# Kernel optimization log

Hardware: AMD Instinct MI355X
Metric: run time of the kernel (lower is better)

Reference implementation:

```python
import jax, jax.numpy as jnp
import numpy as np

B, T, N, D = 2, 16, 512, 256
HID, HEADS = 256, 8
HD = HID // HEADS // 2  # 16
SCALE = HD ** -0.5
LAMBDA_INIT = 0.8 - 0.6 * float(np.exp(-0.3 * (2 - 1)))  # layer_idx = 2
LN_EPS = 1e-5


def setup_inputs() -> dict:
    key = jax.random.key(0)
    ks = jax.random.split(key, 8)
    return {
        "x": jax.random.normal(ks[0], (B, T, N, D), dtype=jnp.float32),
        "Wq": jax.random.normal(ks[1], (D, HID), dtype=jnp.float32) * (D ** -0.5),
        "Wk": jax.random.normal(ks[2], (D, HID), dtype=jnp.float32) * (D ** -0.5),
        "Wv": jax.random.normal(ks[3], (D, HID), dtype=jnp.float32) * (D ** -0.5),
        "lq1": jax.random.normal(ks[4], (HD,), dtype=jnp.float32) * 0.1,
        "lk1": jax.random.normal(ks[5], (HD,), dtype=jnp.float32) * 0.1,
        "lq2": jax.random.normal(ks[6], (HD,), dtype=jnp.float32) * 0.1,
        "lk2": jax.random.normal(ks[7], (HD,), dtype=jnp.float32) * 0.1,
        "ln_gamma": jnp.ones((2 * HD,), dtype=jnp.float32),
        "ln_beta": jnp.zeros((2 * HD,), dtype=jnp.float32),
    }


def _attn_pair(q, k, v1, v2):
    # q,k,v*: [BT, N, H, HD]; shared softmax applied to both value halves
    p = jax.nn.softmax(jnp.einsum('bnhd,bmhd->bhnm', q, k) * SCALE, axis=-1)
    o1 = jnp.einsum('bhnm,bmhd->bnhd', p, v1)
    o2 = jnp.einsum('bhnm,bmhd->bnhd', p, v2)
    return jnp.concatenate([o1, o2], axis=-1)  # [BT, N, H, 2*HD]


def reference(x, Wq, Wk, Wv, lq1, lk1, lq2, lk2, ln_gamma, ln_beta):
    b, t, n, d = x.shape
    # 1x1 Conv2d over channel dim == per-token linear projection
    q = jnp.einsum('btnd,dh->btnh', x, Wq).reshape(b * t, n, HEADS, 2 * HD)
    k = jnp.einsum('btnd,dh->btnh', x, Wk).reshape(b * t, n, HEADS, 2 * HD)
    v = jnp.einsum('btnd,dh->btnh', x, Wv).reshape(b * t, n, HEADS, 2 * HD)
    q1, q2 = jnp.split(q, 2, axis=-1)
    k1, k2 = jnp.split(k, 2, axis=-1)
    v1, v2 = jnp.split(v, 2, axis=-1)
    attn1 = _attn_pair(q1, k1, v1, v2)
    attn2 = _attn_pair(q2, k2, v1, v2)
    lam = jnp.exp(jnp.sum(lq1 * lk1)) - jnp.exp(jnp.sum(lq2 * lk2)) + LAMBDA_INIT
    y = attn1 - lam * attn2  # [BT, N, H, 2*HD]
    mu = jnp.mean(y, axis=-1, keepdims=True)
    var = jnp.mean(jnp.square(y - mu), axis=-1, keepdims=True)
    y = (y - mu) * jax.lax.rsqrt(var + LN_EPS) * ln_gamma + ln_beta
    y = y * (1.0 - LAMBDA_INIT)
    return y.reshape(b, t, n, HEADS * 2 * HD)
```

## Files before the change

kernel.cpp:

```cpp
#include <hip/hip_runtime.h>
#include <cmath>

typedef unsigned short u16;
typedef unsigned int   u32;
typedef __attribute__((ext_vector_type(8))) short short8;
typedef __attribute__((ext_vector_type(4))) float f32x4;

constexpr int BT    = 32;
constexpr int NTOK  = 512;
constexpr int DIM   = 256;
constexpr int HID   = 256;
constexpr int M_ROWS = BT * NTOK;
constexpr int HM     = M_ROWS * 32;
constexpr size_t TENS = (size_t)M_ROWS * HID;
constexpr float LAMBDA_INIT  = 0.35550906759096927f;
constexpr float ONE_MINUS_LI = 0.6444909324090307f;
constexpr float LN_EPS = 1e-5f;
constexpr float QSCALE = 0.36067376022224085f;

constexpr int KCHUNK = 128;

#define MFMA16(a, b, c) __builtin_amdgcn_mfma_f32_16x16x32_bf16((a), (b), (c), 0, 0, 0)
#define LDS_FENCE() asm volatile("" ::: "memory")

__device__ __forceinline__ u16 f2bf(float f) {
    u32 u = __float_as_uint(f);
    return (u16)((u + 0x7FFFu + ((u >> 16) & 1u)) >> 16);
}

__device__ __forceinline__ float fexp2(float x) {
#if defined(__has_builtin) && __has_builtin(__builtin_amdgcn_exp2f)
    return __builtin_amdgcn_exp2f(x);
#else
    return exp2f(x);
#endif
}

__device__ __forceinline__ u32 pack_bf16(float a, float b) {
    u32 ua = __float_as_uint(a) + 0x8000u;
    u32 ub = __float_as_uint(b) + 0x8000u;
    return __builtin_amdgcn_perm(ub, ua, 0x07060302u);
}

__global__ __launch_bounds__(256) void prep_w(const float* __restrict__ Wq,
                                              const float* __restrict__ Wk,
                                              const float* __restrict__ Wv,
                                              u16* __restrict__ Wt) {
    const float* W = (blockIdx.z == 0) ? Wq : (blockIdx.z == 1) ? Wk : Wv;
    u16* dst = Wt + (size_t)blockIdx.z * 65536;
    __shared__ float T[64][65];
    const int k0 = blockIdx.x * 64, n0 = blockIdx.y * 64;
    const int tr = threadIdx.x >> 4;
    const int tc = threadIdx.x & 15;
    #pragma unroll
    for (int i = 0; i < 4; ++i) {
        int row = tr + i * 16;
        float4 v = *(const float4*)&W[(size_t)(k0 + row) * HID + n0 + tc * 4];
        T[row][tc * 4 + 0] = v.x; T[row][tc * 4 + 1] = v.y;
        T[row][tc * 4 + 2] = v.z; T[row][tc * 4 + 3] = v.w;
    }
    __syncthreads();
    #pragma unroll
    for (int i = 0; i < 4; ++i) {
        int n = tr + i * 16;
        int k4 = tc * 4;
        uint2 pk;
        pk.x = (u32)f2bf(T[k4 + 0][n]) | ((u32)f2bf(T[k4 + 1][n]) << 16);
        pk.y = (u32)f2bf(T[k4 + 2][n]) | ((u32)f2bf(T[k4 + 3][n]) << 16);
        *(uint2*)&dst[(size_t)(n0 + n) * DIM + k0 + k4] = pk;
    }
}

__global__ __launch_bounds__(256, 3) void proj_kernel(
    const float* __restrict__ x, const u16* __restrict__ Wt,
    u16* __restrict__ Qh, u16* __restrict__ Kh, u16* __restrict__ Vh)
{
    __shared__ u16 As[64 * 72];
    __shared__ u16 Bs[3][64 * 72];

    const int tid  = threadIdx.x;
    const int m0   = blockIdx.x * 64;
    const int n0   = blockIdx.y * 64;
    const int lane = tid & 63;
    const int wv   = tid >> 6;
    const int q16  = lane & 15;
    const int quad = lane >> 4;
    const int mw   = (wv >> 1) * 32;
    const int nw   = (wv & 1) * 32;

    const int sr = tid >> 2;
    const int sc = (tid & 3) * 16;

    f32x4 acc[3][4];
    #pragma unroll
    for (int z = 0; z < 3; ++z)
        #pragma unroll
        for (int t = 0; t < 4; ++t)
            acc[z][t] = (f32x4){0.f, 0.f, 0.f, 0.f};

    for (int kk = 0; kk < DIM; kk += 64) {
        {
            const float4* xs = (const float4*)&x[(size_t)(m0 + sr) * DIM + kk + sc];
            float4 g0 = xs[0], g1 = xs[1], g2 = xs[2], g3 = xs[3];
            uint4 o0, o1;
            o0.x = (u32)f2bf(g0.x) | ((u32)f2bf(g0.y) << 16);
            o0.y = (u32)f2bf(g0.z) | ((u32)f2bf(g0.w) << 16);
            o0.z = (u32)f2bf(g1.x) | ((u32)f2bf(g1.y) << 16);
            o0.w = (u32)f2bf(g1.z) | ((u32)f2bf(g1.w) << 16);
            o1.x = (u32)f2bf(g2.x) | ((u32)f2bf(g2.y) << 16);
            o1.y = (u32)f2bf(g2.z) | ((u32)f2bf(g2.w) << 16);
            o1.z = (u32)f2bf(g3.x) | ((u32)f2bf(g3.y) << 16);
            o1.w = (u32)f2bf(g3.z) | ((u32)f2bf(g3.w) << 16);
            *(uint4*)&As[sr * 72 + sc]     = o0;
            *(uint4*)&As[sr * 72 + sc + 8] = o1;
        }
        #pragma unroll
        for (int z = 0; z < 3; ++z) {
            const uint4* ws4 = (const uint4*)&Wt[(size_t)z * 65536 + (size_t)(n0 + sr) * DIM + kk + sc];
            *(uint4*)&Bs[z][sr * 72 + sc]     = ws4[0];
            *(uint4*)&Bs[z][sr * 72 + sc + 8] = ws4[1];
        }
        __syncthreads();
        #pragma unroll
        for (int kc = 0; kc < 2; ++kc) {
            short8 a0 = *(const short8*)&As[(mw +      q16) * 72 + kc * 32 + quad * 8];
            short8 a1 = *(const short8*)&As[(mw + 16 + q16) * 72 + kc * 32 + quad * 8];
            #pragma unroll
            for (int z = 0; z < 3; ++z) {
                short8 b0 = *(const short8*)&Bs[z][(nw +      q16) * 72 + kc * 32 + quad * 8];
                short8 b1 = *(const short8*)&Bs[z][(nw + 16 + q16) * 72 + kc * 32 + quad * 8];
                acc[z][0] = MFMA16(a0, b0, acc[z][0]);
                acc[z][1] = MFMA16(a0, b1, acc[z][1]);
                acc[z][2] = MFMA16(a1, b0, acc[z][2]);
                acc[z][3] = MFMA16(a1, b1, acc[z][3]);
            }
        }
        __syncthreads();
    }

    const int hcol = (n0 + nw) >> 5;
    #pragma unroll
    for (int z = 0; z < 3; ++z) {
        u16* C = (z == 0) ? Qh : (z == 1) ? Kh : Vh;
        u16* base = C + (size_t)hcol * HM;
        const float s = (z == 0) ? QSCALE : 1.0f;
        #pragma unroll
        for (int r = 0; r < 4; ++r) {
            const int row = m0 + mw + quad * 4 + r;
            base[(size_t)row * 32 + q16]             = f2bf(acc[z][0][r] * s);
            base[(size_t)row * 32 + q16 + 16]        = f2bf(acc[z][1][r] * s);
            base[(size_t)(row + 16) * 32 + q16]      = f2bf(acc[z][2][r] * s);
            base[(size_t)(row + 16) * 32 + q16 + 16] = f2bf(acc[z][3][r] * s);
        }
    }
}

__global__ __launch_bounds__(256, 3) void attn_kernel(
    const u16* __restrict__ Qh, const u16* __restrict__ Kh, const u16* __restrict__ Vh,
    const float* __restrict__ lq1, const float* __restrict__ lk1,
    const float* __restrict__ lq2, const float* __restrict__ lk2,
    const float* __restrict__ gamma, const float* __restrict__ beta,
    float* __restrict__ out)
{
    constexpr int VSTR = KCHUNK + 8;
    constexpr int NKC  = KCHUNK / 32;

    __shared__ u16 Ks[KCHUNK * 40];
    __shared__ u16 Vts[32 * VSTR];
    __shared__ u16 Pbuf[4][2][2][16 * 40];

    const int qh  = blockIdx.x;
    const int h   = blockIdx.y;
    const int bt  = blockIdx.z;
    const int tid = threadIdx.x;
    const int lane = tid & 63;
    const int wv   = tid >> 6;
    const int q16  = lane & 15;
    const int quad = lane >> 4;

    float sa = 0.f, sb = 0.f;
    #pragma unroll
    for (int d = 0; d < 16; ++d) { sa += lq1[d] * lk1[d]; sb += lq2[d] * lk2[d]; }
    const float lam = __expf(sa) - __expf(sb) + LAMBDA_INIT;

    short8 qv[2];
    #pragma unroll
    for (int qbi = 0; qbi < 2; ++qbi) {
        const int qrow = bt * NTOK + qh * 128 + (qbi * 4 + wv) * 16 + q16;
        qv[qbi] = *(const short8*)(Qh + (size_t)h * HM + (size_t)qrow * 32 + quad * 8);
    }

    const short8 z8 = {0, 0, 0, 0, 0, 0, 0, 0};
    const f32x4  z4 = {0.f, 0.f, 0.f, 0.f};
    const short8 ones8 = {(short)0x3F80, (short)0x3F80, (short)0x3F80, (short)0x3F80,
                          (short)0x3F80, (short)0x3F80, (short)0x3F80, (short)0x3F80};

    f32x4 o1lo[2], o1hi[2], o2lo[2], o2hi[2];
    f32x4 accl1[2], accl2[2];
    #pragma unroll
    for (int qbi = 0; qbi < 2; ++qbi) {
        o1lo[qbi] = z4; o1hi[qbi] = z4; o2lo[qbi] = z4; o2hi[qbi] = z4;
        accl1[qbi] = z4; accl2[qbi] = z4;
    }

    for (int chunk = 0; chunk < NTOK / KCHUNK; ++chunk) {
        if (chunk) __syncthreads();
        {
            const int key  = tid >> 1;
            const int half = (tid & 1) * 16;
            const uint4* src = (const uint4*)(Kh + (size_t)h * HM +
                                (size_t)(bt * NTOK + chunk * KCHUNK + key) * 32 + half);
            uint4* dst = (uint4*)&Ks[key * 40 + half];
            dst[0] = src[0]; dst[1] = src[1];
        }
        {
            const int pr = tid >> 2;
            const int qd = tid & 3;
            const int j0 = pr * 2;
            const u16* v0 = Vh + (size_t)h * HM + (size_t)(bt * NTOK + chunk * KCHUNK + j0) * 32;
            union U { uint4 q4; u32 w[4]; } ra, rb;
            ra.q4 = ((const uint4*)v0)[qd];
            rb.q4 = ((const uint4*)(v0 + 32))[qd];
            #pragma unroll
            for (int k = 0; k < 4; ++k) {
                const int w = qd * 4 + k;
                u32 lo = __builtin_amdgcn_perm(rb.w[k], ra.w[k], 0x05040100u);
                u32 hi = __builtin_amdgcn_perm(rb.w[k], ra.w[k], 0x07060302u);
                *(u32*)&Vts[(2 * w)     * VSTR + j0] = lo;
                *(u32*)&Vts[(2 * w + 1) * VSTR + j0] = hi;
            }
        }
        __syncthreads();

        #pragma unroll
        for (int qbi = 0; qbi < 2; ++qbi) {
            const short8 A1 = (lane < 32) ? qv[qbi] : z8;
            const short8 A2 = (lane < 32) ? z8 : qv[qbi];

            #pragma unroll
            for (int kc = 0; kc < NKC; ++kc) {
                #pragma unroll
                for (int sub = 0; sub < 2; ++sub) {
                    const int key0 = kc * 32 + sub * 16;
                    short8 kf = *(const short8*)&Ks[(key0 + q16) * 40 + quad * 8];
                    __builtin_amdgcn_s_setprio(1);
                    f32x4 s1 = MFMA16(kf, A1, z4);
                    f32x4 s2 = MFMA16(kf, A2, z4);
                    __builtin_amdgcn_s_setprio(0);
                    float p0 = fexp2(s1[0]), p1 = fexp2(s1[1]);
                    float p2 = fexp2(s1[2]), p3 = fexp2(s1[3]);
                    uint2 w1; w1.x = pack_bf16(p0, p1); w1.y = pack_bf16(p2, p3);
                    *(uint2*)&Pbuf[wv][kc & 1][0][q16 * 40 + sub * 16 + quad * 4] = w1;
                    float r0 = fexp2(s2[0]), r1 = fexp2(s2[1]);
                    float r2 = fexp2(s2[2]), r3 = fexp2(s2[3]);
                    uint2 w2; w2.x = pack_bf16(r0, r1); w2.y = pack_bf16(r2, r3);
                    *(uint2*)&Pbuf[wv][kc & 1][1][q16 * 40 + sub * 16 + quad * 4] = w2;
                }
                LDS_FENCE();
                if (kc > 0) {
                    const int pk = kc - 1;
                    const int pb = (kc - 1) & 1;
                    short8 pf1 = *(const short8*)&Pbuf[wv][pb][0][q16 * 40 + quad * 8];
                    short8 pf2 = *(const short8*)&Pbuf[wv][pb][1][q16 * 40 + quad * 8];
                    short8 vlo = *(const short8*)&Vts[q16        * VSTR + pk * 32 + quad * 8];
                    short8 vhi = *(const short8*)&Vts[(16 + q16) * VSTR + pk * 32 + quad * 8];
                    __builtin_amdgcn_s_setprio(1);
                    o1lo[qbi] = MFMA16(pf1, vlo, o1lo[qbi]);
                    o1hi[qbi] = MFMA16(pf1, vhi, o1hi[qbi]);
                    o2lo[qbi] = MFMA16(pf2, vlo, o2lo[qbi]);
                    o2hi[qbi] = MFMA16(pf2, vhi, o2hi[qbi]);
                    accl1[qbi] = MFMA16(pf1, ones8, accl1[qbi]);
                    accl2[qbi] = MFMA16(pf2, ones8, accl2[qbi]);
                    __builtin_amdgcn_s_setprio(0);
                }
                LDS_FENCE();
            }
            {
                const int pk = NKC - 1;
                const int pb = (NKC - 1) & 1;
                short8 pf1 = *(const short8*)&Pbuf[wv][pb][0][q16 * 40 + quad * 8];
                short8 pf2 = *(const short8*)&Pbuf[wv][pb][1][q16 * 40 + quad * 8];
                short8 vlo = *(const short8*)&Vts[q16        * VSTR + pk * 32 + quad * 8];
                short8 vhi = *(const short8*)&Vts[(16 + q16) * VSTR + pk * 32 + quad * 8];
                __builtin_amdgcn_s_setprio(1);
                o1lo[qbi] = MFMA16(pf1, vlo, o1lo[qbi]);
                o1hi[qbi] = MFMA16(pf1, vhi, o1hi[qbi]);
                o2lo[qbi] = MFMA16(pf2, vlo, o2lo[qbi]);
                o2hi[qbi] = MFMA16(pf2, vhi, o2hi[qbi]);
                accl1[qbi] = MFMA16(pf1, ones8, accl1[qbi]);
                accl2[qbi] = MFMA16(pf2, ones8, accl2[qbi]);
                __builtin_amdgcn_s_setprio(0);
            }
            LDS_FENCE();
        }
    }

    const float g_lo = gamma[q16],      g_hi = gamma[16 + q16];
    const float b_lo = beta[q16],       b_hi = beta[16 + q16];

    #pragma unroll
    for (int qbi = 0; qbi < 2; ++qbi) {
        #pragma unroll
        for (int r = 0; r < 4; ++r) {
            const float i1 = 1.0f / accl1[qbi][r];
            const float i2 = 1.0f / accl2[qbi][r];
            const float ylo = o1lo[qbi][r] * i1 - lam * (o2lo[qbi][r] * i2);
            const float yhi = o1hi[qbi][r] * i1 - lam * (o2hi[qbi][r] * i2);

            float s  = ylo + yhi;
            float s2 = ylo * ylo + yhi * yhi;
            #pragma unroll
            for (int off = 1; off < 16; off <<= 1) {
                s  += __shfl_xor(s,  off);
                s2 += __shfl_xor(s2, off);
            }
            const float mu   = s * (1.0f / 32.0f);
            const float var  = s2 * (1.0f / 32.0f) - mu * mu;
            const float rstd = rsqrtf(var + LN_EPS);

            const int row = bt * NTOK + qh * 128 + (qbi * 4 + wv) * 16 + quad * 4 + r;
            float* orow = out + (size_t)row * HID + h * 32;
            orow[q16]      = ((ylo - mu) * rstd * g_lo + b_lo) * ONE_MINUS_LI;
            orow[16 + q16] = ((yhi - mu) * rstd * g_hi + b_hi) * ONE_MINUS_LI;
        }
    }
}

extern "C" void kernel_launch(void* const* d_in, const int* in_sizes, int n_in,
                              void* d_out, int out_size, void* d_ws, size_t ws_size,
                              hipStream_t stream) {
    const float* x   = (const float*)d_in[0];
    const float* Wq  = (const float*)d_in[1];
    const float* Wk  = (const float*)d_in[2];
    const float* Wv  = (const float*)d_in[3];
    const float* lq1 = (const float*)d_in[4];
    const float* lk1 = (const float*)d_in[5];
    const float* lq2 = (const float*)d_in[6];
    const float* lk2 = (const float*)d_in[7];
    const float* gam = (const float*)d_in[8];
    const float* bet = (const float*)d_in[9];
    float* out = (float*)d_out;

    u16* ws = (u16*)d_ws;
    u16* Wt = ws;
    u16* Qh = Wt + 3 * 65536;
    u16* Kh = Qh + TENS;
    u16* Vh = Kh + TENS;

    hipLaunchKernelGGL(prep_w, dim3(4, 4, 3), dim3(256), 0, stream, Wq, Wk, Wv, Wt);
    hipLaunchKernelGGL(proj_kernel, dim3(M_ROWS / 64, HID / 64), dim3(256), 0, stream,
                       x, Wt, Qh, Kh, Vh);
    hipLaunchKernelGGL(attn_kernel, dim3(4, 8, 32), dim3(256), 0, stream,
                       Qh, Kh, Vh, lq1, lk1, lq2, lk2, gam, bet, out);
}
```

Baseline: 130.7 us.

## Double-buffer K/V chunks in LDS with warp-specialized loads

Halves the key chunk size to 64 and double-buffers the K and transposed-V tiles in shared memory. Half the threads load K and the other half load and transpose V. The next chunk is loaded after the current chunk's compute, and there is one barrier per chunk instead of two. The intent is to cut barrier stalls and overlap global loads with MFMA work. In exchange there are more chunk iterations, and the loads are issued after compute rather than before it, so the overlap may be limited.

```diff
diff --git a/kernel.cpp b/kernel.cpp
--- a/kernel.cpp
+++ b/kernel.cpp
@@ -18,7 +18,7 @@
 constexpr float LN_EPS = 1e-5f;
 constexpr float QSCALE = 0.36067376022224085f;
 
-constexpr int KCHUNK = 128;
+constexpr int KCHUNK = 64;
 
 #define MFMA16(a, b, c) __builtin_amdgcn_mfma_f32_16x16x32_bf16((a), (b), (c), 0, 0, 0)
 #define LDS_FENCE() asm volatile("" ::: "memory")
@@ -164,9 +164,12 @@
 {
     constexpr int VSTR = KCHUNK + 8;
     constexpr int NKC  = KCHUNK / 32;
-
-    __shared__ u16 Ks[KCHUNK * 40];
-    __shared__ u16 Vts[32 * VSTR];
+    constexpr int NCH  = NTOK / KCHUNK;
+    constexpr int KS_ELE = KCHUNK * 40;
+    constexpr int VT_ELE = 32 * VSTR;
+
+    __shared__ u16 Ks[2 * KS_ELE];
+    __shared__ u16 Vts[2 * VT_ELE];
     __shared__ u16 Pbuf[4][2][2][16 * 40];
 
     const int qh  = blockIdx.x;
@@ -203,34 +206,39 @@
         accl1[qbi] = z4; accl2[qbi] = z4;
     }
 
-    for (int chunk = 0; chunk < NTOK / KCHUNK; ++chunk) {
-        if (chunk) __syncthreads();
-        {
-            const int key  = tid >> 1;
-            const int half = (tid & 1) * 16;
-            const uint4* src = (const uint4*)(Kh + (size_t)h * HM +
-                                (size_t)(bt * NTOK + chunk * KCHUNK + key) * 32 + half);
-            uint4* dst = (uint4*)&Ks[key * 40 + half];
-            dst[0] = src[0]; dst[1] = src[1];
-        }
-        {
-            const int pr = tid >> 2;
-            const int qd = tid & 3;
-            const int j0 = pr * 2;
-            const u16* v0 = Vh + (size_t)h * HM + (size_t)(bt * NTOK + chunk * KCHUNK + j0) * 32;
-            union U { uint4 q4; u32 w[4]; } ra, rb;
-            ra.q4 = ((const uint4*)v0)[qd];
-            rb.q4 = ((const uint4*)(v0 + 32))[qd];
-            #pragma unroll
-            for (int k = 0; k < 4; ++k) {
-                const int w = qd * 4 + k;
-                u32 lo = __builtin_amdgcn_perm(rb.w[k], ra.w[k], 0x05040100u);
-                u32 hi = __builtin_amdgcn_perm(rb.w[k], ra.w[k], 0x07060302u);
-                *(u32*)&Vts[(2 * w)     * VSTR + j0] = lo;
-                *(u32*)&Vts[(2 * w + 1) * VSTR + j0] = hi;
-            }
-        }
-        __syncthreads();
+    const u16* Kbase = Kh + (size_t)h * HM + (size_t)(bt * NTOK) * 32;
+    const u16* Vbase = Vh + (size_t)h * HM + (size_t)(bt * NTOK) * 32;
+
+    if (tid < 128) {
+        const int key  = tid >> 1;
+        const int half = (tid & 1) * 16;
+        const uint4* src = (const uint4*)(Kbase + (size_t)key * 32 + half);
+        uint4* dst = (uint4*)&Ks[key * 40 + half];
+        dst[0] = src[0]; dst[1] = src[1];
+    } else {
+        const int vt = tid - 128;
+        const int pr = vt >> 2;
+        const int qd = vt & 3;
+        const int j0 = pr * 2;
+        const u16* v0 = Vbase + (size_t)j0 * 32;
+        union U { uint4 q4; u32 w[4]; } ra, rb;
+        ra.q4 = ((const uint4*)v0)[qd];
+        rb.q4 = ((const uint4*)(v0 + 32))[qd];
+        #pragma unroll
+        for (int k = 0; k < 4; ++k) {
+            const int w = qd * 4 + k;
+            u32 lo = __builtin_amdgcn_perm(rb.w[k], ra.w[k], 0x05040100u);
+            u32 hi = __builtin_amdgcn_perm(rb.w[k], ra.w[k], 0x07060302u);
+            *(u32*)&Vts[(2 * w)     * VSTR + j0] = lo;
+            *(u32*)&Vts[(2 * w + 1) * VSTR + j0] = hi;
+        }
+    }
+    __syncthreads();
+
+    for (int chunk = 0; chunk < NCH; ++chunk) {
+        const int cb = chunk & 1;
+        const u16* ksb = &Ks[cb * KS_ELE];
+        const u16* vtb = &Vts[cb * VT_ELE];
 
         #pragma unroll
         for (int qbi = 0; qbi < 2; ++qbi) {
@@ -242,7 +250,7 @@
                 #pragma unroll
                 for (int sub = 0; sub < 2; ++sub) {
                     const int key0 = kc * 32 + sub * 16;
-                    short8 kf = *(const short8*)&Ks[(key0 + q16) * 40 + quad * 8];
+                    short8 kf = *(const short8*)&ksb[(key0 + q16) * 40 + quad * 8];
                     __builtin_amdgcn_s_setprio(1);
                     f32x4 s1 = MFMA16(kf, A1, z4);
                     f32x4 s2 = MFMA16(kf, A2, z4);
@@ -262,8 +270,8 @@
                     const int pb = (kc - 1) & 1;
                     short8 pf1 = *(const short8*)&Pbuf[wv][pb][0][q16 * 40 + quad * 8];
                     short8 pf2 = *(const short8*)&Pbuf[wv][pb][1][q16 * 40 + quad * 8];
-                    short8 vlo = *(const short8*)&Vts[q16        * VSTR + pk * 32 + quad * 8];
-                    short8 vhi = *(const short8*)&Vts[(16 + q16) * VSTR + pk * 32 + quad * 8];
+                    short8 vlo = *(const short8*)&vtb[q16        * VSTR + pk * 32 + quad * 8];
+                    short8 vhi = *(const short8*)&vtb[(16 + q16) * VSTR + pk * 32 + quad * 8];
                     __builtin_amdgcn_s_setprio(1);
                     o1lo[qbi] = MFMA16(pf1, vlo, o1lo[qbi]);
                     o1hi[qbi] = MFMA16(pf1, vhi, o1hi[qbi]);
@@ -280,8 +288,8 @@
                 const int pb = (NKC - 1) & 1;
                 short8 pf1 = *(const short8*)&Pbuf[wv][pb][0][q16 * 40 + quad * 8];
                 short8 pf2 = *(const short8*)&Pbuf[wv][pb][1][q16 * 40 + quad * 8];
-                short8 vlo = *(const short8*)&Vts[q16        * VSTR + pk * 32 + quad * 8];
-                short8 vhi = *(const short8*)&Vts[(16 + q16) * VSTR + pk * 32 + quad * 8];
+                short8 vlo = *(const short8*)&vtb[q16        * VSTR + pk * 32 + quad * 8];
+                short8 vhi = *(const short8*)&vtb[(16 + q16) * VSTR + pk * 32 + quad * 8];
                 __builtin_amdgcn_s_setprio(1);
                 o1lo[qbi] = MFMA16(pf1, vlo, o1lo[qbi]);
                 o1hi[qbi] = MFMA16(pf1, vhi, o1hi[qbi]);
@@ -293,6 +301,35 @@
             }
             LDS_FENCE();
         }
+
+        if (chunk < NCH - 1) {
+            const size_t coff = (size_t)(chunk + 1) * KCHUNK * 32;
+            if (tid < 128) {
+                const int key  = tid >> 1;
+                const int half = (tid & 1) * 16;
+                const uint4* src = (const uint4*)(Kbase + coff + (size_t)key * 32 + half);
+                uint4* dst = (uint4*)&Ks[(cb ^ 1) * KS_ELE + key * 40 + half];
+                dst[0] = src[0]; dst[1] = src[1];
+            } else {
+                const int vt = tid - 128;
+                const int pr = vt >> 2;
+                const int qd = vt & 3;
+                const int j0 = pr * 2;
+                const u16* v0 = Vbase + coff + (size_t)j0 * 32;
+                union U { uint4 q4; u32 w[4]; } ra, rb;
+                ra.q4 = ((const uint4*)v0)[qd];
+                rb.q4 = ((const uint4*)(v0 + 32))[qd];
+                #pragma unroll
+                for (int k = 0; k < 4; ++k) {
+                    const int w = qd * 4 + k;
+                    u32 lo = __builtin_amdgcn_perm(rb.w[k], ra.w[k], 0x05040100u);
+                    u32 hi = __builtin_amdgcn_perm(rb.w[k], ra.w[k], 0x07060302u);
+                    *(u32*)&Vts[(cb ^ 1) * VT_ELE + (2 * w)     * VSTR + j0] = lo;
+                    *(u32*)&Vts[(cb ^ 1) * VT_ELE + (2 * w + 1) * VSTR + j0] = hi;
+                }
+            }
+        }
+        __syncthreads();
     }
 
     const float g_lo = gamma[q16],      g_hi = gamma[16 + q16];
```

Result: no change. 133.0 us (+1.8%).
